# Kernel tuning notes

Hardware: AMD Instinct MI355X
Metric: run time of the kernel (lower is better)

## Reference

```python
import jax, jax.numpy as jnp
import numpy as np
import math

B, N, E, D = 8, 2048, 2048, 128
MAX_K = 8
HYPER_DIM = 128
LN_EPS = 1e-5


def _sinusoidal_pe(max_pos, dim):
    pe = np.zeros((max_pos, dim), dtype=np.float32)
    position = np.arange(max_pos, dtype=np.float32)[:, None]
    div_term = np.exp(np.arange(0, dim, 2, dtype=np.float32) * (-math.log(10000.0) / dim))
    pe[:, 0::2] = np.sin(position * div_term)
    pe[:, 1::2] = np.cos(position * div_term)
    return jnp.asarray(pe)


def setup_inputs() -> dict:
    key = jax.random.key(0)
    ks = jax.random.split(key, 24)
    s = 0.05
    inp = {
        'x_v': jax.random.normal(ks[0], (B, N, D), jnp.float32),
        'x_e': jax.random.normal(ks[1], (B, E, D), jnp.float32),
        'incidence': (jax.random.uniform(ks[2], (B, N, E), jnp.float32) < 0.01).astype(jnp.float32),
        'suffix_normalizer': jax.random.uniform(ks[3], (B, N), jnp.float32) * 20.0,
        'edge_orders': 1 + jax.random.randint(ks[4], (B, E), 0, MAX_K),
        'node_mask': jax.random.randint(ks[5], (B, N), 0, 2) > 0,
        'edge_mask': jax.random.randint(ks[6], (B, E), 0, 2) > 0,
        'pe1_table': _sinusoidal_pe(MAX_K + 1, D),
        'pe2_table': _sinusoidal_pe(2, D),
        'bias_b': jax.random.uniform(ks[7], (1, D), jnp.float32, -1, 1) / math.sqrt(D),
    }
    i = 8
    for m in ('mlp1', 'mlp2', 'mlp3'):
        inp[m + '_W1'] = jax.random.normal(ks[i], (D, HYPER_DIM), jnp.float32) * s; i += 1
        inp[m + '_b1'] = jnp.zeros((HYPER_DIM,), jnp.float32)
        inp[m + '_W2'] = jax.random.normal(ks[i], (HYPER_DIM, D), jnp.float32) * s; i += 1
        inp[m + '_b2'] = jnp.zeros((D,), jnp.float32)
    for n in ('norm1', 'norm2', 'norm3'):
        inp[n + '_g'] = jnp.ones((D,), jnp.float32)
        inp[n + '_b'] = jnp.zeros((D,), jnp.float32)
    return inp


def _ln(x, g, b):
    mu = jnp.mean(x, axis=-1, keepdims=True)
    var = jnp.mean(jnp.square(x - mu), axis=-1, keepdims=True)
    return (x - mu) * jax.lax.rsqrt(var + LN_EPS) * g + b


def _mlp(x, W1, b1, W2, b2):
    return jax.nn.relu(x @ W1 + b1) @ W2 + b2


def reference(x_v, x_e, incidence, suffix_normalizer, edge_orders, node_mask, edge_mask,
              pe1_table, pe2_table, bias_b,
              mlp1_W1, mlp1_b1, mlp1_W2, mlp1_b2,
              mlp2_W1, mlp2_b1, mlp2_W2, mlp2_b2,
              mlp3_W1, mlp3_b1, mlp3_W2, mlp3_b2,
              norm1_g, norm1_b, norm2_g, norm2_b, norm3_g, norm3_b):
    nm = node_mask[..., None]  # [B,N,1]
    em = edge_mask[..., None]  # [B,E,1]
    x_v = jnp.where(nm, x_v, 0.0)
    x_e = jnp.where(em, x_e, 0.0)
    pe1_k1 = pe1_table[1][None, None, :]          # [1,1,D]
    pe1_k = pe1_table[edge_orders]                # [B,E,D]
    x_v = x_v + _mlp(_ln(x_v, norm1_g, norm1_b) + pe1_k1, mlp1_W1, mlp1_b1, mlp1_W2, mlp1_b2)
    x_e = x_e + _mlp(_ln(x_e, norm1_g, norm1_b) + pe1_k, mlp1_W1, mlp1_b1, mlp1_W2, mlp1_b2)
    x_v = jnp.where(nm, x_v, 0.0)
    x_e = jnp.where(em, x_e, 0.0)
    agg = jnp.einsum('bne,bed->bnd', incidence, x_e)
    x1 = x_v + agg / (1.0 + suffix_normalizer[..., None])
    pe2_s1 = pe2_table[1][None, None, :]
    x1 = x1 + _mlp(_ln(x1, norm2_g, norm2_b) + pe2_s1, mlp2_W1, mlp2_b1, mlp2_W2, mlp2_b2)
    x = jnp.where(nm, x1, 0.0)
    x = x + _mlp(_ln(x, norm3_g, norm3_b), mlp3_W1, mlp3_b1, mlp3_W2, mlp3_b2)
    x = x + bias_b
    x = jnp.where(nm, x, 0.0)
    return x
```

## Files before the change

kernel.cpp:

```cpp
#include <hip/hip_runtime.h>
#include <stdint.h>

#define BB 8
#define NN 2048
#define EE 2048
#define DD 128
#define RBP 132
#define NTHREADS 256
#define WMAT_U32 8192
#define SCANB 2048
#define LCAP 64

typedef __attribute__((ext_vector_type(8))) short bf16x8;
typedef __attribute__((ext_vector_type(4))) float f32x4;

__device__ inline unsigned bf16rne(float f) {
    unsigned u = __float_as_uint(f);
    return (u + 0x7fffu + ((u >> 16) & 1u)) >> 16;
}
__device__ inline float bf16lo(unsigned u) { return __uint_as_float(u << 16); }
__device__ inline float bf16hi(unsigned u) { return __uint_as_float(u & 0xffff0000u); }

#define SWZ(b) ((b) ^ ((((b) >> 8) & 7) << 4))

struct __align__(16) SmemK1 {
    float rowbuf[32][RBP];
    unsigned h[32 * DD / 2];
    unsigned scw[4][64];
    int rmask[32];
    int ords[32];
};

struct __align__(16) SmemK2 {
    float rowbuf[16][RBP];
    unsigned h[16 * DD / 2];
    int rmask[16];
};

__device__ inline void load_rows32(SmemK1& s, const float* __restrict__ src,
                                   const int* __restrict__ mask) {
    int t = threadIdx.x;
    for (int idx = t; idx < 32 * 32; idx += NTHREADS) {
        int r = idx >> 5, c4 = (idx & 31) * 4;
        float4 v = make_float4(0.f, 0.f, 0.f, 0.f);
        if (mask[r] != 0) v = *(const float4*)&src[r * DD + c4];
        *(float4*)&s.rowbuf[r][c4] = v;
    }
    __syncthreads();
}

__device__ inline void ln32(SmemK1& s, const float* __restrict__ gw,
                            const float* __restrict__ bw,
                            const float* __restrict__ pe_base, bool per_row_pe) {
    int t = threadIdx.x;
    int gr = t >> 3, g = t & 7;
    int base = g * 16;
    float x[16];
    float4* xp = (float4*)x;
    xp[0] = *(const float4*)&s.rowbuf[gr][base + 0];
    xp[1] = *(const float4*)&s.rowbuf[gr][base + 4];
    xp[2] = *(const float4*)&s.rowbuf[gr][base + 8];
    xp[3] = *(const float4*)&s.rowbuf[gr][base + 12];
    float s1 = 0.f, s2 = 0.f;
    #pragma unroll
    for (int i = 0; i < 16; i++) { s1 += x[i]; s2 += x[i] * x[i]; }
    #pragma unroll
    for (int off = 1; off < 8; off <<= 1) {
        s1 += __shfl_xor(s1, off, 64);
        s2 += __shfl_xor(s2, off, 64);
    }
    float mu = s1 * (1.f / 128.f);
    float var = s2 * (1.f / 128.f) - mu * mu;
    float rstd = rsqrtf(var + 1e-5f);
    const float* pe = nullptr;
    if (pe_base) pe = per_row_pe ? (pe_base + (size_t)s.ords[gr] * DD) : pe_base;
    unsigned p[8];
    #pragma unroll
    for (int j = 0; j < 8; j++) {
        int k0 = base + 2 * j;
        float v0 = (x[2 * j] - mu) * rstd * gw[k0] + bw[k0];
        float v1 = (x[2 * j + 1] - mu) * rstd * gw[k0 + 1] + bw[k0 + 1];
        if (pe) { v0 += pe[k0]; v1 += pe[k0 + 1]; }
        p[j] = bf16rne(v0) | (bf16rne(v1) << 16);
    }
    char* hb = (char*)s.h;
    int byte0 = gr * 256 + g * 32;
    uint4 lo = make_uint4(p[0], p[1], p[2], p[3]);
    uint4 hi = make_uint4(p[4], p[5], p[6], p[7]);
    *(uint4*)(hb + SWZ(byte0)) = lo;
    *(uint4*)(hb + SWZ(byte0 + 16)) = hi;
    __syncthreads();
}

template <bool TO_H>
__device__ inline void mm32_f32w(SmemK1& s, const float* __restrict__ Wf,
                                 const float* __restrict__ bias) {
    int t = threadIdx.x;
    int w = t >> 6, l = t & 63;
    int lm = l & 15, lk = l >> 4;
    bf16x8 bfr[2][4];
    #pragma unroll
    for (int nbl = 0; nbl < 2; nbl++) {
        int n = w * 32 + nbl * 16 + lm;
        #pragma unroll
        for (int kb = 0; kb < 4; kb++) {
            int k0 = kb * 32 + lk * 8;
            unsigned pk[4];
            #pragma unroll
            for (int jp = 0; jp < 4; jp++) {
                float a = Wf[(size_t)(k0 + 2 * jp) * DD + n];
                float b = Wf[(size_t)(k0 + 2 * jp + 1) * DD + n];
                pk[jp] = bf16rne(a) | (bf16rne(b) << 16);
            }
            uint4 u = make_uint4(pk[0], pk[1], pk[2], pk[3]);
            bfr[nbl][kb] = *(bf16x8*)&u;
        }
    }
    const char* hb = (const char*)s.h;
    bf16x8 afr[2][4];
    #pragma unroll
    for (int mb = 0; mb < 2; mb++) {
        int row = mb * 16 + lm;
        #pragma unroll
        for (int kb = 0; kb < 4; kb++)
            afr[mb][kb] = *(const bf16x8*)(hb + SWZ(row * 256 + kb * 64 + lk * 16));
    }
    f32x4 acc[2][2];
    #pragma unroll
    for (int mb = 0; mb < 2; mb++)
        #pragma unroll
        for (int nbl = 0; nbl < 2; nbl++)
            acc[mb][nbl] = (f32x4){0.f, 0.f, 0.f, 0.f};
    #pragma unroll
    for (int kb = 0; kb < 4; kb++)
        #pragma unroll
        for (int mb = 0; mb < 2; mb++)
            #pragma unroll
            for (int nbl = 0; nbl < 2; nbl++)
                acc[mb][nbl] = __builtin_amdgcn_mfma_f32_16x16x32_bf16(
                    afr[mb][kb], bfr[nbl][kb], acc[mb][nbl], 0, 0, 0);
    float bcol0 = bias[w * 32 + lm];
    float bcol1 = bias[w * 32 + 16 + lm];
    __syncthreads();
    if (TO_H) {
        char* hw = (char*)s.h;
        #pragma unroll
        for (int mb = 0; mb < 2; mb++)
            #pragma unroll
            for (int nbl = 0; nbl < 2; nbl++) {
                int col = w * 32 + nbl * 16 + lm;
                float bc = nbl ? bcol1 : bcol0;
                #pragma unroll
                for (int j = 0; j < 4; j++) {
                    int row = mb * 16 + lk * 4 + j;
                    float v = fmaxf(acc[mb][nbl][j] + bc, 0.f);
                    *(unsigned short*)(hw + SWZ(row * 256 + col * 2)) =
                        (unsigned short)bf16rne(v);
                }
            }
    } else {
        #pragma unroll
        for (int mb = 0; mb < 2; mb++)
            #pragma unroll
            for (int nbl = 0; nbl < 2; nbl++) {
                int col = w * 32 + nbl * 16 + lm;
                float bc = nbl ? bcol1 : bcol0;
                #pragma unroll
                for (int j = 0; j < 4; j++) {
                    int row = mb * 16 + lk * 4 + j;
                    s.rowbuf[row][col] += acc[mb][nbl][j] + bc;
                }
            }
    }
    __syncthreads();
}

__device__ inline void scan_rows(SmemK1& s, const float* __restrict__ inc,
                                 const int* __restrict__ nmask,
                                 unsigned* __restrict__ lists, int* __restrict__ cnts,
                                 int wid, int nwaves) {
    int l = threadIdx.x & 63;
    int w = threadIdx.x >> 6;
    unsigned* sc = s.scw[w];
    unsigned long long lmlt = (1ull << l) - 1ull;
    for (int grow = wid; grow < BB * NN; grow += nwaves) {
        if (nmask[grow] == 0) continue;
        const float4* ir = (const float4*)(inc + (size_t)grow * EE);
        float4 v[8];
        #pragma unroll
        for (int i = 0; i < 8; i++) v[i] = ir[l + 64 * i];
        int total = 0;
        #pragma unroll
        for (int i = 0; i < 8; i++) {
            #pragma unroll
            for (int c = 0; c < 4; c++) {
                float val = (c == 0) ? v[i].x : (c == 1) ? v[i].y : (c == 2) ? v[i].z : v[i].w;
                bool nz = (val != 0.f);
                unsigned long long msk = __ballot(nz);
                if (nz) {
                    int pos = total + __popcll(msk & lmlt);
                    if (pos < LCAP) sc[pos] = (unsigned)((l + 64 * i) * 4 + c);
                }
                total += __popcll(msk);
            }
        }
        if (total > LCAP) total = LCAP;
        asm volatile("s_waitcnt lgkmcnt(0)" ::: "memory");
        if (l < 16) {
            uint4 q = *(const uint4*)&sc[4 * l];
            *(uint4*)&lists[(size_t)grow * LCAP + 4 * l] = q;
        }
        if (l == 0) cnts[grow] = total;
    }
}

__device__ inline void ln16(SmemK2& s, const float* __restrict__ gw,
                            const float* __restrict__ bw,
                            const float* __restrict__ pe) {
    int t = threadIdx.x;
    int gr = t >> 4, g = t & 15;
    int base = g * 8;
    float x[8];
    float4* xp = (float4*)x;
    xp[0] = *(const float4*)&s.rowbuf[gr][base + 0];
    xp[1] = *(const float4*)&s.rowbuf[gr][base + 4];
    float s1 = 0.f, s2 = 0.f;
    #pragma unroll
    for (int i = 0; i < 8; i++) { s1 += x[i]; s2 += x[i] * x[i]; }
    #pragma unroll
    for (int off = 1; off < 16; off <<= 1) {
        s1 += __shfl_xor(s1, off, 64);
        s2 += __shfl_xor(s2, off, 64);
    }
    float mu = s1 * (1.f / 128.f);
    float var = s2 * (1.f / 128.f) - mu * mu;
    float rstd = rsqrtf(var + 1e-5f);
    unsigned p[4];
    #pragma unroll
    for (int j = 0; j < 4; j++) {
        int k0 = base + 2 * j;
        float v0 = (x[2 * j] - mu) * rstd * gw[k0] + bw[k0];
        float v1 = (x[2 * j + 1] - mu) * rstd * gw[k0 + 1] + bw[k0 + 1];
        if (pe) { v0 += pe[k0]; v1 += pe[k0 + 1]; }
        p[j] = bf16rne(v0) | (bf16rne(v1) << 16);
    }
    char* hb = (char*)s.h;
    uint4 q = make_uint4(p[0], p[1], p[2], p[3]);
    *(uint4*)(hb + SWZ(gr * 256 + g * 16)) = q;
    __syncthreads();
}

template <bool TO_H>
__device__ inline void mm16(SmemK2& s, const unsigned* __restrict__ WT,
                            const float* __restrict__ bias) {
    int t = threadIdx.x;
    int w = t >> 6, l = t & 63;
    int lm = l & 15, lk = l >> 4;
    bf16x8 bfr[2][4];
    const uint4* wt4 = (const uint4*)WT;
    #pragma unroll
    for (int nbl = 0; nbl < 2; nbl++) {
        int n = w * 32 + nbl * 16 + lm;
        #pragma unroll
        for (int kb = 0; kb < 4; kb++) {
            uint4 u = wt4[n * 16 + kb * 4 + lk];
            bfr[nbl][kb] = *(bf16x8*)&u;
        }
    }
    const char* hb = (const char*)s.h;
    bf16x8 afr[4];
    #pragma unroll
    for (int kb = 0; kb < 4; kb++)
        afr[kb] = *(const bf16x8*)(hb + SWZ(lm * 256 + kb * 64 + lk * 16));
    f32x4 acc[2];
    acc[0] = (f32x4){0.f, 0.f, 0.f, 0.f};
    acc[1] = (f32x4){0.f, 0.f, 0.f, 0.f};
    #pragma unroll
    for (int kb = 0; kb < 4; kb++)
        #pragma unroll
        for (int nbl = 0; nbl < 2; nbl++)
            acc[nbl] = __builtin_amdgcn_mfma_f32_16x16x32_bf16(
                afr[kb], bfr[nbl][kb], acc[nbl], 0, 0, 0);
    float bcol0 = bias[w * 32 + lm];
    float bcol1 = bias[w * 32 + 16 + lm];
    __syncthreads();
    if (TO_H) {
        char* hw = (char*)s.h;
        #pragma unroll
        for (int nbl = 0; nbl < 2; nbl++) {
            int col = w * 32 + nbl * 16 + lm;
            float bc = nbl ? bcol1 : bcol0;
            #pragma unroll
            for (int j = 0; j < 4; j++) {
                int row = lk * 4 + j;
                float v = fmaxf(acc[nbl][j] + bc, 0.f);
                *(unsigned short*)(hw + SWZ(row * 256 + col * 2)) =
                    (unsigned short)bf16rne(v);
            }
        }
    } else {
        #pragma unroll
        for (int nbl = 0; nbl < 2; nbl++) {
            int col = w * 32 + nbl * 16 + lm;
            float bc = nbl ? bcol1 : bcol0;
            #pragma unroll
            for (int j = 0; j < 4; j++) {
                int row = lk * 4 + j;
                s.rowbuf[row][col] += acc[nbl][j] + bc;
            }
        }
    }
    __syncthreads();
}

__device__ inline void gather16(SmemK2& s, int row0,
                                const unsigned* __restrict__ lists,
                                const int* __restrict__ cnts,
                                const unsigned* __restrict__ e2b,
                                const float* __restrict__ sn) {
    int t = threadIdx.x;
    int w = t >> 6, l = t & 63;
    #pragma unroll
    for (int i = 0; i < 4; i++) {
        int r = w * 4 + i;
        if (s.rmask[r] == 0) continue;
        int grow = row0 + r;
        int cnt = cnts[grow];
        unsigned pk = (l < cnt) ? lists[(size_t)grow * LCAP + l] : 0u;
        float ax = 0.f, ay = 0.f;
        for (int j0 = 0; j0 < cnt; j0 += 8) {
            int nn = cnt - j0;
            unsigned uv[8];
            #pragma unroll
            for (int u = 0; u < 8; u++) {
                unsigned e = __shfl(pk, j0 + u, 64);
                uv[u] = (u < nn) ? e2b[(size_t)e * 64 + l] : 0u;
            }
            #pragma unroll
            for (int u = 0; u < 8; u++) { ax += bf16lo(uv[u]); ay += bf16hi(uv[u]); }
        }
        float inv = 1.f / (1.f + sn[grow]);
        float2* rb = (float2*)&s.rowbuf[r][2 * l];
        float2 cur = *rb;
        cur.x += ax * inv;
        cur.y += ay * inv;
        *rb = cur;
    }
    __syncthreads();
}

__global__ __launch_bounds__(NTHREADS) void k1_kernel(
    const float* __restrict__ x_e, const int* __restrict__ emask,
    const int* __restrict__ nmask, const int* __restrict__ eord,
    const float* __restrict__ pe1, const float* __restrict__ inc,
    const float* __restrict__ n1g, const float* __restrict__ n1b,
    const float* __restrict__ W11, const float* __restrict__ b11,
    const float* __restrict__ W12, const float* __restrict__ b12,
    const float* __restrict__ W21, const float* __restrict__ W22,
    const float* __restrict__ W31, const float* __restrict__ W32,
    unsigned* __restrict__ WT, unsigned* __restrict__ e2pk,
    unsigned* __restrict__ lists, int* __restrict__ cnts) {
    __shared__ SmemK1 s;
    int bid = blockIdx.x;
    int t = threadIdx.x;
    if (bid < SCANB) {
        int gtid = bid * NTHREADS + t;
        if (gtid < 6 * WMAT_U32) {
            int mat = gtid >> 13;
            int idx = gtid & (WMAT_U32 - 1);
            int n = idx >> 6, j = idx & 63;
            const float* W = mat == 0 ? W11 : mat == 1 ? W12 : mat == 2 ? W21
                           : mat == 3 ? W22 : mat == 4 ? W31 : W32;
            float a = W[(2 * j) * DD + n];
            float b = W[(2 * j + 1) * DD + n];
            WT[gtid] = bf16rne(a) | (bf16rne(b) << 16);
        }
        int wid = bid * 4 + (t >> 6);
        scan_rows(s, inc, nmask, lists, cnts, wid, SCANB * 4);
        return;
    }
    int lb = bid - SCANB;
    int bb = lb & 7;
    int e0 = (lb >> 3) * 32;
    int rowbase = bb * EE + e0;
    if (t < 32) {
        s.rmask[t] = emask[rowbase + t];
        int o = eord[rowbase + t];
        s.ords[t] = o < 0 ? 0 : (o > 8 ? 8 : o);
    }
    load_rows32(s, x_e + (size_t)rowbase * DD, emask + rowbase);
    ln32(s, n1g, n1b, pe1, true);
    mm32_f32w<true>(s, W11, b11);
    mm32_f32w<false>(s, W12, b12);
    unsigned* dst = e2pk + (size_t)rowbase * (DD / 2);
    for (int idx = t; idx < 32 * 16; idx += NTHREADS) {
        int r = idx >> 4, q = idx & 15;
        uint4 o = make_uint4(0u, 0u, 0u, 0u);
        if (s.rmask[r] != 0) {
            const float* rp = &s.rowbuf[r][q * 8];
            o.x = bf16rne(rp[0]) | (bf16rne(rp[1]) << 16);
            o.y = bf16rne(rp[2]) | (bf16rne(rp[3]) << 16);
            o.z = bf16rne(rp[4]) | (bf16rne(rp[5]) << 16);
            o.w = bf16rne(rp[6]) | (bf16rne(rp[7]) << 16);
        }
        *(uint4*)&dst[r * 64 + q * 4] = o;
    }
}

__global__ __launch_bounds__(NTHREADS) void k2_kernel(
    const float* __restrict__ x_v, const int* __restrict__ nmask,
    const float* __restrict__ sn,
    const float* __restrict__ pe1, const float* __restrict__ pe2,
    const float* __restrict__ biasb,
    const float* __restrict__ n1g, const float* __restrict__ n1b,
    const float* __restrict__ n2g, const float* __restrict__ n2b,
    const float* __restrict__ n3g, const float* __restrict__ n3b,
    const unsigned* __restrict__ WT,
    const float* __restrict__ b11, const float* __restrict__ b12,
    const float* __restrict__ b21, const float* __restrict__ b22,
    const float* __restrict__ b31, const float* __restrict__ b32,
    const unsigned* __restrict__ e2pk, const unsigned* __restrict__ lists,
    const int* __restrict__ cnts, float* __restrict__ out) {
    __shared__ SmemK2 s;
    int bid = blockIdx.x;
    int bb = bid & 7;
    int n0 = (bid >> 3) * 16;
    int row0 = bb * NN + n0;
    int t = threadIdx.x;
    if (t < 16) s.rmask[t] = nmask[row0 + t];
    __syncthreads();
    for (int idx = t; idx < 16 * 32; idx += NTHREADS) {
        int r = idx >> 5, c4 = (idx & 31) * 4;
        float4 v = make_float4(0.f, 0.f, 0.f, 0.f);
        if (s.rmask[r] != 0) v = *(const float4*)&x_v[(size_t)(row0 + r) * DD + c4];
        *(float4*)&s.rowbuf[r][c4] = v;
    }
    __syncthreads();
    ln16(s, n1g, n1b, pe1 + DD);
    mm16<true>(s, WT + 0 * WMAT_U32, b11);
    mm16<false>(s, WT + 1 * WMAT_U32, b12);
    gather16(s, row0, lists, cnts, e2pk + (size_t)bb * (EE * (DD / 2)), sn);
    ln16(s, n2g, n2b, pe2 + DD);
    mm16<true>(s, WT + 2 * WMAT_U32, b21);
    mm16<false>(s, WT + 3 * WMAT_U32, b22);
    ln16(s, n3g, n3b, nullptr);
    mm16<true>(s, WT + 4 * WMAT_U32, b31);
    mm16<false>(s, WT + 5 * WMAT_U32, b32);
    for (int idx = t; idx < 16 * 32; idx += NTHREADS) {
        int r = idx >> 5, c4 = (idx & 31) * 4;
        float4 v = make_float4(0.f, 0.f, 0.f, 0.f);
        if (s.rmask[r] != 0) {
            v = *(const float4*)&s.rowbuf[r][c4];
            float4 bbv = *(const float4*)&biasb[c4];
            v.x += bbv.x; v.y += bbv.y; v.z += bbv.z; v.w += bbv.w;
        }
        *(float4*)&out[(size_t)(row0 + r) * DD + c4] = v;
    }
}

extern "C" void kernel_launch(void* const* d_in, const int* in_sizes, int n_in,
                              void* d_out, int out_size, void* d_ws, size_t ws_size,
                              hipStream_t stream) {
    const float* x_v   = (const float*)d_in[0];
    const float* x_e   = (const float*)d_in[1];
    const float* inc   = (const float*)d_in[2];
    const float* sn    = (const float*)d_in[3];
    const int*   eord  = (const int*)d_in[4];
    const int*   nmask = (const int*)d_in[5];
    const int*   emask = (const int*)d_in[6];
    const float* pe1   = (const float*)d_in[7];
    const float* pe2   = (const float*)d_in[8];
    const float* biasb = (const float*)d_in[9];
    const float* W11   = (const float*)d_in[10];
    const float* b11   = (const float*)d_in[11];
    const float* W12   = (const float*)d_in[12];
    const float* b12   = (const float*)d_in[13];
    const float* W21   = (const float*)d_in[14];
    const float* b21   = (const float*)d_in[15];
    const float* W22   = (const float*)d_in[16];
    const float* b22   = (const float*)d_in[17];
    const float* W31   = (const float*)d_in[18];
    const float* b31   = (const float*)d_in[19];
    const float* W32   = (const float*)d_in[20];
    const float* b32   = (const float*)d_in[21];
    const float* n1g   = (const float*)d_in[22];
    const float* n1b   = (const float*)d_in[23];
    const float* n2g   = (const float*)d_in[24];
    const float* n2b   = (const float*)d_in[25];
    const float* n3g   = (const float*)d_in[26];
    const float* n3b   = (const float*)d_in[27];

    unsigned* e2pk  = (unsigned*)d_ws;
    unsigned* WT    = e2pk + (size_t)BB * EE * (DD / 2);
    unsigned* lists = WT + 6 * WMAT_U32;
    int*      cnts  = (int*)(lists + (size_t)BB * NN * LCAP);
    float*    out   = (float*)d_out;

    dim3 blk(NTHREADS);
    k1_kernel<<<dim3(SCANB + BB * EE / 32), blk, 0, stream>>>(
        x_e, emask, nmask, eord, pe1, inc,
        n1g, n1b, W11, b11, W12, b12, W21, W22, W31, W32,
        WT, e2pk, lists, cnts);
    k2_kernel<<<dim3(BB * NN / 16), blk, 0, stream>>>(
        x_v, nmask, sn, pe1, pe2, biasb,
        n1g, n1b, n2g, n2b, n3g, n3b,
        WT, b11, b12, b21, b22, b31, b32,
        e2pk, lists, cnts, out);
}
```

Before: 65.94 us.

## Scan two incidence rows per wave and prefetch gather metadata

The incidence scan is restructured so each wave handles exactly two rows in a single pass. It issues both rows' loads up front and writes the compacted edge lists straight to global memory, dropping the LDS staging buffer and the strided loop. The aim is more loads in flight on the bandwidth-bound incidence read. In the node kernel, the gather loads all four rows' lists, counts and normalizers before the accumulation loop, and the row loads no longer wait on the mask, which is applied afterwards by zeroing masked rows. The trade-offs are scattered global stores for the lists, higher register pressure in the scan, and extra reads of masked rows.

Result: no change. 66.80 us (+1.3%).

```diff
diff --git a/kernel.cpp b/kernel.cpp
--- a/kernel.cpp
+++ b/kernel.cpp
@@ -26,7 +26,6 @@
 struct __align__(16) SmemK1 {
     float rowbuf[32][RBP];
     unsigned h[32 * DD / 2];
-    unsigned scw[4][64];
     int rmask[32];
     int ords[32];
 };
@@ -37,13 +36,11 @@
     int rmask[16];
 };
 
-__device__ inline void load_rows32(SmemK1& s, const float* __restrict__ src,
-                                   const int* __restrict__ mask) {
+__device__ inline void load_rows32(SmemK1& s, const float* __restrict__ src) {
     int t = threadIdx.x;
     for (int idx = t; idx < 32 * 32; idx += NTHREADS) {
         int r = idx >> 5, c4 = (idx & 31) * 4;
-        float4 v = make_float4(0.f, 0.f, 0.f, 0.f);
-        if (mask[r] != 0) v = *(const float4*)&src[r * DD + c4];
+        float4 v = *(const float4*)&src[r * DD + c4];
         *(float4*)&s.rowbuf[r][c4] = v;
     }
     __syncthreads();
@@ -175,42 +172,59 @@
     __syncthreads();
 }
 
-__device__ inline void scan_rows(SmemK1& s, const float* __restrict__ inc,
-                                 const int* __restrict__ nmask,
-                                 unsigned* __restrict__ lists, int* __restrict__ cnts,
-                                 int wid, int nwaves) {
+__device__ inline void scan2(const float* __restrict__ inc,
+                             const int* __restrict__ nmask,
+                             unsigned* __restrict__ lists, int* __restrict__ cnts,
+                             int grow0) {
     int l = threadIdx.x & 63;
-    int w = threadIdx.x >> 6;
-    unsigned* sc = s.scw[w];
     unsigned long long lmlt = (1ull << l) - 1ull;
-    for (int grow = wid; grow < BB * NN; grow += nwaves) {
-        if (nmask[grow] == 0) continue;
-        const float4* ir = (const float4*)(inc + (size_t)grow * EE);
-        float4 v[8];
-        #pragma unroll
-        for (int i = 0; i < 8; i++) v[i] = ir[l + 64 * i];
-        int total = 0;
-        #pragma unroll
-        for (int i = 0; i < 8; i++) {
-            #pragma unroll
-            for (int c = 0; c < 4; c++) {
-                float val = (c == 0) ? v[i].x : (c == 1) ? v[i].y : (c == 2) ? v[i].z : v[i].w;
-                bool nz = (val != 0.f);
-                unsigned long long msk = __ballot(nz);
-                if (nz) {
-                    int pos = total + __popcll(msk & lmlt);
-                    if (pos < LCAP) sc[pos] = (unsigned)((l + 64 * i) * 4 + c);
-                }
-                total += __popcll(msk);
-            }
-        }
-        if (total > LCAP) total = LCAP;
-        asm volatile("s_waitcnt lgkmcnt(0)" ::: "memory");
-        if (l < 16) {
-            uint4 q = *(const uint4*)&sc[4 * l];
-            *(uint4*)&lists[(size_t)grow * LCAP + 4 * l] = q;
-        }
-        if (l == 0) cnts[grow] = total;
+    int m0 = nmask[grow0];
+    int m1 = nmask[grow0 + 1];
+    const float4* ir0 = (const float4*)(inc + (size_t)grow0 * EE);
+    const float4* ir1 = (const float4*)(inc + (size_t)(grow0 + 1) * EE);
+    float4 v0[8], v1[8];
+    if (m0) {
+        #pragma unroll
+        for (int i = 0; i < 8; i++) v0[i] = ir0[l + 64 * i];
+    } else {
+        #pragma unroll
+        for (int i = 0; i < 8; i++) v0[i] = make_float4(0.f, 0.f, 0.f, 0.f);
+    }
+    if (m1) {
+        #pragma unroll
+        for (int i = 0; i < 8; i++) v1[i] = ir1[l + 64 * i];
+    } else {
+        #pragma unroll
+        for (int i = 0; i < 8; i++) v1[i] = make_float4(0.f, 0.f, 0.f, 0.f);
+    }
+    unsigned* lp0 = lists + (size_t)grow0 * LCAP;
+    unsigned* lp1 = lists + (size_t)(grow0 + 1) * LCAP;
+    int t0 = 0, t1 = 0;
+    #pragma unroll
+    for (int i = 0; i < 8; i++) {
+        #pragma unroll
+        for (int c = 0; c < 4; c++) {
+            float a = (c == 0) ? v0[i].x : (c == 1) ? v0[i].y : (c == 2) ? v0[i].z : v0[i].w;
+            float b = (c == 0) ? v1[i].x : (c == 1) ? v1[i].y : (c == 2) ? v1[i].z : v1[i].w;
+            bool na = (a != 0.f), nb = (b != 0.f);
+            unsigned long long ka = __ballot(na);
+            unsigned long long kb = __ballot(nb);
+            unsigned e = (unsigned)((l + 64 * i) * 4 + c);
+            if (na) {
+                int p = t0 + __popcll(ka & lmlt);
+                if (p < LCAP) lp0[p] = e;
+            }
+            if (nb) {
+                int p = t1 + __popcll(kb & lmlt);
+                if (p < LCAP) lp1[p] = e;
+            }
+            t0 += __popcll(ka);
+            t1 += __popcll(kb);
+        }
+    }
+    if (l == 0) {
+        if (m0) cnts[grow0] = t0 > LCAP ? LCAP : t0;
+        if (m1) cnts[grow0 + 1] = t1 > LCAP ? LCAP : t1;
     }
 }
 
@@ -320,26 +334,32 @@
                                 const float* __restrict__ sn) {
     int t = threadIdx.x;
     int w = t >> 6, l = t & 63;
+    int cnt[4]; unsigned pk[4]; float snv[4];
+    #pragma unroll
+    for (int i = 0; i < 4; i++) {
+        int grow = row0 + w * 4 + i;
+        pk[i] = lists[(size_t)grow * LCAP + l];
+        snv[i] = sn[grow];
+        cnt[i] = cnts[grow];
+    }
     #pragma unroll
     for (int i = 0; i < 4; i++) {
         int r = w * 4 + i;
         if (s.rmask[r] == 0) continue;
-        int grow = row0 + r;
-        int cnt = cnts[grow];
-        unsigned pk = (l < cnt) ? lists[(size_t)grow * LCAP + l] : 0u;
+        int cn = cnt[i]; if (cn > LCAP) cn = LCAP;
         float ax = 0.f, ay = 0.f;
-        for (int j0 = 0; j0 < cnt; j0 += 8) {
-            int nn = cnt - j0;
+        for (int j0 = 0; j0 < cn; j0 += 8) {
+            int nn = cn - j0;
             unsigned uv[8];
             #pragma unroll
             for (int u = 0; u < 8; u++) {
-                unsigned e = __shfl(pk, j0 + u, 64);
+                unsigned e = __shfl(pk[i], j0 + u, 64);
                 uv[u] = (u < nn) ? e2b[(size_t)e * 64 + l] : 0u;
             }
             #pragma unroll
             for (int u = 0; u < 8; u++) { ax += bf16lo(uv[u]); ay += bf16hi(uv[u]); }
         }
-        float inv = 1.f / (1.f + sn[grow]);
+        float inv = 1.f / (1.f + snv[i]);
         float2* rb = (float2*)&s.rowbuf[r][2 * l];
         float2 cur = *rb;
         cur.x += ax * inv;
@@ -376,7 +396,7 @@
             WT[gtid] = bf16rne(a) | (bf16rne(b) << 16);
         }
         int wid = bid * 4 + (t >> 6);
-        scan_rows(s, inc, nmask, lists, cnts, wid, SCANB * 4);
+        scan2(inc, nmask, lists, cnts, wid * 2);
         return;
     }
     int lb = bid - SCANB;
@@ -388,7 +408,7 @@
         int o = eord[rowbase + t];
         s.ords[t] = o < 0 ? 0 : (o > 8 ? 8 : o);
     }
-    load_rows32(s, x_e + (size_t)rowbase * DD, emask + rowbase);
+    load_rows32(s, x_e + (size_t)rowbase * DD);
     ln32(s, n1g, n1b, pe1, true);
     mm32_f32w<true>(s, W11, b11);
     mm32_f32w<false>(s, W12, b12);
@@ -428,12 +448,15 @@
     int row0 = bb * NN + n0;
     int t = threadIdx.x;
     if (t < 16) s.rmask[t] = nmask[row0 + t];
-    __syncthreads();
     for (int idx = t; idx < 16 * 32; idx += NTHREADS) {
         int r = idx >> 5, c4 = (idx & 31) * 4;
-        float4 v = make_float4(0.f, 0.f, 0.f, 0.f);
-        if (s.rmask[r] != 0) v = *(const float4*)&x_v[(size_t)(row0 + r) * DD + c4];
+        float4 v = *(const float4*)&x_v[(size_t)(row0 + r) * DD + c4];
         *(float4*)&s.rowbuf[r][c4] = v;
+    }
+    __syncthreads();
+    for (int idx = t; idx < 16 * 32; idx += NTHREADS) {
+        int r = idx >> 5, c4 = (idx & 31) * 4;
+        if (s.rmask[r] == 0) *(float4*)&s.rowbuf[r][c4] = make_float4(0.f, 0.f, 0.f, 0.f);
     }
     __syncthreads();
     ln16(s, n1g, n1b, pe1 + DD);
```
